# Kernel optimization log

Measured on AMD Instinct MI355X. Metric: run time of the kernel, lower is better.

Reference implementation:

```python
import jax, jax.numpy as jnp
import numpy as np
from functools import partial

B, S, D = 64, 1024, 1024
C = 10  # number of chained GRU steps (self.c)


def setup_inputs() -> dict:
    key = jax.random.key(0)
    ks = jax.random.split(key, 8)
    sc = 1.0 / np.sqrt(D)
    return {
        "feat": jax.random.normal(ks[0], (B, S, D), dtype=jnp.float32),
        "a_w": jax.random.normal(ks[1], (D,), dtype=jnp.float32) * sc,          # Linear(D,1,bias=False)
        "W_ih": jax.random.normal(ks[2], (3 * D, D + 1), dtype=jnp.float32) * sc,  # GRU input weights (r,z,n)
        "W_hh": jax.random.normal(ks[3], (3 * D, D), dtype=jnp.float32) * sc,      # GRU hidden weights (r,z,n)
        "b_ih": jax.random.normal(ks[4], (3 * D,), dtype=jnp.float32) * sc,
        "b_hh": jax.random.normal(ks[5], (3 * D,), dtype=jnp.float32) * sc,
        "W_out": jax.random.normal(ks[6], (1, D), dtype=jnp.float32) * sc,         # out_layer Linear(D,1)
        "b_out": jax.random.normal(ks[7], (1,), dtype=jnp.float32) * sc,
    }


def reference(feat, a_w, W_ih, W_hh, b_ih, b_hh, W_out, b_out):
    # Attention pooling: softmax over sequence dim of a scalar score per frame.
    logits = jnp.einsum("bsd,d->bs", feat, a_w)                 # [B, S]
    w = jax.nn.softmax(logits, axis=1)                           # [B, S]
    pooled = jnp.einsum("bs,bsd->bd", w, feat)                  # [B, D]

    def gru_step(carry, _):
        h, score = carry
        x = jnp.concatenate([pooled, score], axis=-1)            # [B, D+1]
        gi = x @ W_ih.T + b_ih                                   # [B, 3D]
        gh = h @ W_hh.T + b_hh                                   # [B, 3D]
        i_r, i_z, i_n = jnp.split(gi, 3, axis=-1)
        h_r, h_z, h_n = jnp.split(gh, 3, axis=-1)
        r = jax.nn.sigmoid(i_r + h_r)
        z = jax.nn.sigmoid(i_z + h_z)
        n = jnp.tanh(i_n + r * h_n)
        h_new = (1.0 - z) * n + z * h
        score_new = jax.nn.sigmoid(h_new @ W_out.T + b_out)      # [B, 1]
        return (h_new, score_new), score_new

    h0 = jnp.zeros_like(pooled)                                  # GRU hidden starts at zero
    s0 = jnp.zeros((pooled.shape[0], 1), dtype=pooled.dtype)     # zero_score initial chain input
    _, scores = jax.lax.scan(gru_step, (h0, s0), None, length=C)  # scores: [C, B, 1]
    out = jnp.transpose(scores[..., 0], (1, 0))                  # [B, C]
    return out
```

## Files before the change

### kernel.cpp

```cpp
#include <hip/hip_runtime.h>
#include <hip/hip_bf16.h>
#include <math.h>

#define B 64
#define S 1024
#define D 1024
#define C 10
#define TD 3072

typedef __attribute__((ext_vector_type(8))) short s8v;
typedef __attribute__((ext_vector_type(4))) float f4v;

__device__ __forceinline__ float wave_sum_bc(float v) {
    #pragma unroll
    for (int off = 1; off < 64; off <<= 1) v += __shfl_xor(v, off, 64);
    return v;
}
__device__ __forceinline__ float sigm(float x) { return 1.0f / (1.0f + expf(-x)); }
__device__ __forceinline__ short f2bf(float f) {
    __hip_bfloat16 h = __float2bfloat16(f);
    return *reinterpret_cast<short*>(&h);
}

__global__ __launch_bounds__(256) void k_pre(const float* __restrict__ feat,
        const float* __restrict__ a_w, const float* __restrict__ W_ih,
        const float* __restrict__ W_hh, float* __restrict__ part, float* __restrict__ ml,
        short* __restrict__ BihP, short* __restrict__ BhhP, float* __restrict__ wscore) {
    __shared__ float sacc[4][1024];
    __shared__ float sml[4][2];
    int n = blockIdx.x, tid = threadIdx.x;

    if (n >= 1024) {
        if (n < 4096) {
            int rel = n - 1024;
            const float* Wsrc = (rel < 1536) ? W_ih : W_hh;
            short* dst = (rel < 1536) ? BihP : BhhP;
            int stride = (rel < 1536) ? (D + 1) : D;
            int rn = (rel < 1536) ? rel : rel - 1536;
            int gid = rn * 256 + tid;
            int fid = gid >> 6, l = gid & 63;
            int s = fid & 31, g = (fid >> 5) % 3, dt = fid / 96;
            int row = g * 1024 + dt * 16 + (l & 15);
            int k0 = s * 32 + ((l >> 4) << 3);
            const float* src = Wsrc + (size_t)row * stride + k0;
            short v[8];
            #pragma unroll
            for (int j = 0; j < 8; ++j) v[j] = f2bf(src[j]);
            short* d = dst + ((size_t)fid * 64 + l) * 8;
            #pragma unroll
            for (int j = 0; j < 8; ++j) d[j] = v[j];
        } else {
            int j = (n - 4096) * 256 + tid;
            wscore[j] = W_ih[(size_t)j * (D + 1) + D];
        }
        return;
    }

    int ch = n & 15, b = n >> 4;
    int w = tid >> 6, lane = tid & 63;
    float4 aw[4], acc[4];
    #pragma unroll
    for (int r = 0; r < 4; ++r) {
        aw[r] = *reinterpret_cast<const float4*>(&a_w[r * 256 + lane * 4]);
        acc[r] = make_float4(0.f, 0.f, 0.f, 0.f);
    }
    float m = -INFINITY, l = 0.f;
    const float* fb = feat + ((size_t)b * S + ch * 64 + w * 16) * D;
    for (int i = 0; i < 16; ++i) {
        float4 f[4];
        #pragma unroll
        for (int r = 0; r < 4; ++r)
            f[r] = *reinterpret_cast<const float4*>(&fb[(size_t)i * D + r * 256 + lane * 4]);
        float dot = 0.f;
        #pragma unroll
        for (int r = 0; r < 4; ++r)
            dot += f[r].x * aw[r].x + f[r].y * aw[r].y + f[r].z * aw[r].z + f[r].w * aw[r].w;
        dot = wave_sum_bc(dot);
        if (dot <= m) {
            float wg = expf(dot - m);
            l += wg;
            #pragma unroll
            for (int r = 0; r < 4; ++r) {
                acc[r].x += wg * f[r].x; acc[r].y += wg * f[r].y;
                acc[r].z += wg * f[r].z; acc[r].w += wg * f[r].w;
            }
        } else {
            float sc = expf(m - dot);
            l = l * sc + 1.f;
            #pragma unroll
            for (int r = 0; r < 4; ++r) {
                acc[r].x = acc[r].x * sc + f[r].x; acc[r].y = acc[r].y * sc + f[r].y;
                acc[r].z = acc[r].z * sc + f[r].z; acc[r].w = acc[r].w * sc + f[r].w;
            }
            m = dot;
        }
    }
    #pragma unroll
    for (int r = 0; r < 4; ++r)
        *reinterpret_cast<float4*>(&sacc[w][r * 256 + lane * 4]) = acc[r];
    if (lane == 0) { sml[w][0] = m; sml[w][1] = l; }
    __syncthreads();
    float m0 = sml[0][0], m1 = sml[1][0], m2 = sml[2][0], m3 = sml[3][0];
    float mg = fmaxf(fmaxf(m0, m1), fmaxf(m2, m3));
    float s0 = expf(m0 - mg), s1 = expf(m1 - mg), s2 = expf(m2 - mg), s3 = expf(m3 - mg);
    int c = tid * 4;
    float4 a0 = *reinterpret_cast<float4*>(&sacc[0][c]);
    float4 a1 = *reinterpret_cast<float4*>(&sacc[1][c]);
    float4 a2 = *reinterpret_cast<float4*>(&sacc[2][c]);
    float4 a3 = *reinterpret_cast<float4*>(&sacc[3][c]);
    float4 o;
    o.x = s0 * a0.x + s1 * a1.x + s2 * a2.x + s3 * a3.x;
    o.y = s0 * a0.y + s1 * a1.y + s2 * a2.y + s3 * a3.y;
    o.z = s0 * a0.z + s1 * a1.z + s2 * a2.z + s3 * a3.z;
    o.w = s0 * a0.w + s1 * a1.w + s2 * a2.w + s3 * a3.w;
    *reinterpret_cast<float4*>(&part[((size_t)b * 16 + ch) * D + c]) = o;
    if (tid == 0) {
        float lg = s0 * sml[0][1] + s1 * sml[1][1] + s2 * sml[2][1] + s3 * sml[3][1];
        ml[(b * 16 + ch) * 2] = mg;
        ml[(b * 16 + ch) * 2 + 1] = lg;
    }
}

__global__ __launch_bounds__(256) void k_mid(const float* __restrict__ part,
        const float* __restrict__ ml, short* __restrict__ pooledP) {
    int b = blockIdx.x, tid = threadIdx.x;
    float mg = -INFINITY;
    #pragma unroll
    for (int q = 0; q < 16; ++q) mg = fmaxf(mg, ml[(b * 16 + q) * 2]);
    float denom = 0.f, sc[16];
    #pragma unroll
    for (int q = 0; q < 16; ++q) {
        sc[q] = expf(ml[(b * 16 + q) * 2] - mg);
        denom += sc[q] * ml[(b * 16 + q) * 2 + 1];
    }
    float inv = 1.f / denom;
    int c = tid * 4;
    float4 o = make_float4(0.f, 0.f, 0.f, 0.f);
    #pragma unroll
    for (int q = 0; q < 16; ++q) {
        float4 p = *reinterpret_cast<const float4*>(&part[((size_t)b * 16 + q) * D + c]);
        o.x += sc[q] * p.x; o.y += sc[q] * p.y; o.z += sc[q] * p.z; o.w += sc[q] * p.w;
    }
    float ov[4] = {o.x * inv, o.y * inv, o.z * inv, o.w * inv};
    int m = b >> 4;
    #pragma unroll
    for (int j4 = 0; j4 < 4; ++j4) {
        int d = c + j4;
        int s = d >> 5, lane2 = (b & 15) + (((d >> 3) & 3) << 4), jj = d & 7;
        pooledP[(((size_t)m * 32 + s) * 64 + lane2) * 8 + jj] = f2bf(ov[j4]);
    }
}

__global__ __launch_bounds__(512) void k_step(const s8v* __restrict__ Bp,
        const s8v* __restrict__ Ain, short* __restrict__ Aout, float* __restrict__ hf,
        float* __restrict__ gi0, const float* __restrict__ wscore,
        const float* __restrict__ b_ih, const float* __restrict__ b_hh,
        const float* __restrict__ W_out, const float* __restrict__ b_out,
        float* __restrict__ spart, float* __restrict__ out, int t) {
    __shared__ float psum[8][16][49];
    __shared__ float sredS[16][17];
    __shared__ float sredO[16][17];
    int tid = threadIdx.x, w = tid >> 6, l = tid & 63;
    int n = blockIdx.x, xcd = n & 7, slot = n >> 3;
    int dt = xcd * 8 + (slot & 7), bh = slot >> 3;
    int bq0 = bh * 16;
    int lb = tid & 15, c = (tid >> 4) & 15;
    bool epi = (tid < 256);
    int b = bq0 + lb, d = dt * 16 + c;

    float e_bo = 0.f, e_b0 = 0.f, e_b1 = 0.f, e_b2 = 0.f, e_wo = 0.f;
    float e_i0 = 0.f, e_i1 = 0.f, e_i2 = 0.f;
    float e_w0 = 0.f, e_w1 = 0.f, e_w2 = 0.f, e_hf = 0.f;
    if (epi) {
        e_bo = b_out[0];
        e_b0 = b_hh[d]; e_b1 = b_hh[D + d]; e_b2 = b_hh[2 * D + d];
        e_wo = W_out[d];
        if (t == 0) {
            e_i0 = b_ih[d]; e_i1 = b_ih[D + d]; e_i2 = b_ih[2 * D + d];
        } else {
            e_i0 = gi0[(size_t)b * TD + d];
            e_i1 = gi0[(size_t)b * TD + D + d];
            e_i2 = gi0[(size_t)b * TD + 2 * D + d];
            e_w0 = wscore[d]; e_w1 = wscore[D + d]; e_w2 = wscore[2 * D + d];
            e_hf = hf[(size_t)b * D + d];
            const float* sp = spart + ((size_t)(t - 1) * B + b) * 64 + c * 4;
            sredS[lb][c] = sp[0] + sp[1] + sp[2] + sp[3];
        }
    }

    f4v acc[3];
    #pragma unroll
    for (int g = 0; g < 3; ++g) acc[g] = (f4v){0.f, 0.f, 0.f, 0.f};
    #pragma unroll
    for (int s8 = 0; s8 < 4; ++s8) {
        int s = w * 4 + s8;
        s8v a  = Ain[((size_t)bh * 32 + s) * 64 + l];
        s8v b0 = Bp[((size_t)(dt * 3 + 0) * 32 + s) * 64 + l];
        s8v b1 = Bp[((size_t)(dt * 3 + 1) * 32 + s) * 64 + l];
        s8v b2 = Bp[((size_t)(dt * 3 + 2) * 32 + s) * 64 + l];
        acc[0] = __builtin_amdgcn_mfma_f32_16x16x32_bf16(a, b0, acc[0], 0, 0, 0);
        acc[1] = __builtin_amdgcn_mfma_f32_16x16x32_bf16(a, b1, acc[1], 0, 0, 0);
        acc[2] = __builtin_amdgcn_mfma_f32_16x16x32_bf16(a, b2, acc[2], 0, 0, 0);
    }
    #pragma unroll
    for (int g = 0; g < 3; ++g)
        #pragma unroll
        for (int r = 0; r < 4; ++r)
            psum[w][(l >> 4) * 4 + r][g * 16 + (l & 15)] = acc[g][r];
    __syncthreads();

    if (epi) {
        float g3[3];
        #pragma unroll
        for (int g = 0; g < 3; ++g) {
            int c48 = g * 16 + c;
            float v = 0.f;
            #pragma unroll
            for (int ww = 0; ww < 8; ++ww) v += psum[ww][lb][c48];
            g3[g] = v;
        }
        float gir, giz, gin, ghr, ghz, ghn, hprev;
        if (t == 0) {
            gir = g3[0] + e_i0;
            giz = g3[1] + e_i1;
            gin = g3[2] + e_i2;
            gi0[(size_t)b * TD + d] = gir;
            gi0[(size_t)b * TD + D + d] = giz;
            gi0[(size_t)b * TD + 2 * D + d] = gin;
            ghr = e_b0; ghz = e_b1; ghn = e_b2;
            hprev = 0.f;
        } else {
            float ssum = e_bo;
            #pragma unroll
            for (int q = 0; q < 16; ++q) ssum += sredS[lb][q];
            float score = sigm(ssum);
            if (dt == 0 && c == 0) out[b * C + (t - 1)] = score;
            gir = e_i0 + score * e_w0;
            giz = e_i1 + score * e_w1;
            gin = e_i2 + score * e_w2;
            ghr = e_b0 + g3[0];
            ghz = e_b1 + g3[1];
            ghn = e_b2 + g3[2];
            hprev = e_hf;
        }
        float rr = sigm(gir + ghr);
        float zz = sigm(giz + ghz);
        float nn = tanhf(gin + rr * ghn);
        float hnew = (1.f - zz) * nn + zz * hprev;
        hf[(size_t)b * D + d] = hnew;
        int s = d >> 5, lane2 = (b & 15) + (((d >> 3) & 3) << 4), jj = d & 7;
        Aout[(((size_t)bh * 32 + s) * 64 + lane2) * 8 + jj] = f2bf(hnew);
        sredO[lb][c] = hnew * e_wo;
    }
    __syncthreads();
    if (tid < 16) {
        float v = 0.f;
        #pragma unroll
        for (int q = 0; q < 16; ++q) v += sredO[tid][q];
        spart[((size_t)t * B + bq0 + tid) * 64 + dt] = v;
    }
}

__global__ void k_final(const float* __restrict__ spart, const float* __restrict__ b_out,
                        float* __restrict__ out) {
    int b = threadIdx.x;
    float s = b_out[0];
    const float* sp = spart + ((size_t)(C - 1) * B + b) * 64;
    #pragma unroll
    for (int k = 0; k < 64; ++k) s += sp[k];
    out[b * C + (C - 1)] = sigm(s);
}

extern "C" void kernel_launch(void* const* d_in, const int* in_sizes, int n_in,
                              void* d_out, int out_size, void* d_ws, size_t ws_size,
                              hipStream_t stream) {
    const float* feat  = (const float*)d_in[0];
    const float* a_w   = (const float*)d_in[1];
    const float* W_ih  = (const float*)d_in[2];
    const float* W_hh  = (const float*)d_in[3];
    const float* b_ih  = (const float*)d_in[4];
    const float* b_hh  = (const float*)d_in[5];
    const float* W_out = (const float*)d_in[6];
    const float* b_out = (const float*)d_in[7];
    float* out = (float*)d_out;
    float* ws = (float*)d_ws;

    float* part    = ws;
    float* ml      = part + (size_t)B * 16 * D;
    float* gi0     = ml + B * 16 * 2;
    float* hf      = gi0 + (size_t)B * TD;
    float* spart   = hf + B * D;
    float* wscore  = spart + (size_t)C * B * 64;
    short* pooledP = (short*)(wscore + TD);
    short* hpA     = pooledP + (size_t)B * D;
    short* hpB     = hpA + (size_t)B * D;
    short* BihP    = hpB + (size_t)B * D;
    short* BhhP    = BihP + (size_t)D * TD;

    k_pre<<<dim3(4108), 256, 0, stream>>>(feat, a_w, W_ih, W_hh, part, ml,
                                          BihP, BhhP, wscore);
    k_mid<<<dim3(64), 256, 0, stream>>>(part, ml, pooledP);
    k_step<<<dim3(256), 512, 0, stream>>>((const s8v*)BihP, (const s8v*)pooledP, hpA,
                                          hf, gi0, wscore, b_ih, b_hh, W_out, b_out,
                                          spart, out, 0);
    for (int t = 1; t < C; ++t) {
        short* ain = (t & 1) ? hpA : hpB;
        short* aout = (t & 1) ? hpB : hpA;
        k_step<<<dim3(256), 512, 0, stream>>>((const s8v*)BhhP, (const s8v*)ain, aout,
                                              hf, gi0, wscore, b_ih, b_hh, W_out, b_out,
                                              spart, out, t);
    }
    k_final<<<dim3(1), 64, 0, stream>>>(spart, b_out, out);
}
```

Before: 116.6 us.

## Fuse GRU step launches into one persistent kernel with atomic grid barriers

Replaces the ten per-step k_step launches and k_final with a single persistent kernel. Blocks synchronize through per-batch-group atomic counters and spin-wait instead of kernel boundaries. W_hh fragments stay in registers across steps, and gi and h stay in LDS instead of being reread from global memory. This removes launch overhead and repeated weight loads. It relies on all 256 blocks being co-resident and on relaxed atomics giving enough ordering, so it risks deadlock or stale reads.

```diff
diff --git a/kernel.cpp b/kernel.cpp
--- a/kernel.cpp
+++ b/kernel.cpp
@@ -10,6 +10,7 @@
 
 typedef __attribute__((ext_vector_type(8))) short s8v;
 typedef __attribute__((ext_vector_type(4))) float f4v;
+typedef unsigned long long u64;
 
 __device__ __forceinline__ float wave_sum_bc(float v) {
     #pragma unroll
@@ -21,11 +22,24 @@
     __hip_bfloat16 h = __float2bfloat16(f);
     return *reinterpret_cast<short*>(&h);
 }
+__device__ __forceinline__ u64 aload64(u64* p) {
+    return __hip_atomic_load(p, __ATOMIC_RELAXED, __HIP_MEMORY_SCOPE_AGENT);
+}
+__device__ __forceinline__ void astore64(u64* p, u64 v) {
+    __hip_atomic_store(p, v, __ATOMIC_RELAXED, __HIP_MEMORY_SCOPE_AGENT);
+}
+__device__ __forceinline__ float aloadf(float* p) {
+    return __hip_atomic_load(p, __ATOMIC_RELAXED, __HIP_MEMORY_SCOPE_AGENT);
+}
+__device__ __forceinline__ void astoref(float* p, float v) {
+    __hip_atomic_store(p, v, __ATOMIC_RELAXED, __HIP_MEMORY_SCOPE_AGENT);
+}
 
 __global__ __launch_bounds__(256) void k_pre(const float* __restrict__ feat,
         const float* __restrict__ a_w, const float* __restrict__ W_ih,
         const float* __restrict__ W_hh, float* __restrict__ part, float* __restrict__ ml,
-        short* __restrict__ BihP, short* __restrict__ BhhP, float* __restrict__ wscore) {
+        short* __restrict__ BihP, short* __restrict__ BhhP, float* __restrict__ wscore,
+        unsigned* __restrict__ bar) {
     __shared__ float sacc[4][1024];
     __shared__ float sml[4][2];
     int n = blockIdx.x, tid = threadIdx.x;
@@ -52,6 +66,7 @@
         } else {
             int j = (n - 4096) * 256 + tid;
             wscore[j] = W_ih[(size_t)j * (D + 1) + D];
+            if (n == 4096 && tid < 64) bar[tid] = 0u;
         }
         return;
     }
@@ -151,15 +166,19 @@
     }
 }
 
-__global__ __launch_bounds__(512) void k_step(const s8v* __restrict__ Bp,
-        const s8v* __restrict__ Ain, short* __restrict__ Aout, float* __restrict__ hf,
-        float* __restrict__ gi0, const float* __restrict__ wscore,
+__global__ __launch_bounds__(512, 2) void k_persist(const s8v* __restrict__ BihP,
+        const s8v* __restrict__ BhhP, const short* __restrict__ pooledP,
+        u64* hpA, u64* hpB, const float* __restrict__ wscore,
         const float* __restrict__ b_ih, const float* __restrict__ b_hh,
         const float* __restrict__ W_out, const float* __restrict__ b_out,
-        float* __restrict__ spart, float* __restrict__ out, int t) {
+        float* spart, float* __restrict__ out, unsigned* bar) {
     __shared__ float psum[8][16][49];
+    __shared__ float gilds[16][49];
+    __shared__ float hl[16][17];
     __shared__ float sredS[16][17];
     __shared__ float sredO[16][17];
+    __shared__ unsigned short hbf[16][16];
+
     int tid = threadIdx.x, w = tid >> 6, l = tid & 63;
     int n = blockIdx.x, xcd = n & 7, slot = n >> 3;
     int dt = xcd * 8 + (slot & 7), bh = slot >> 3;
@@ -167,108 +186,184 @@
     int lb = tid & 15, c = (tid >> 4) & 15;
     bool epi = (tid < 256);
     int b = bq0 + lb, d = dt * 16 + c;
-
-    float e_bo = 0.f, e_b0 = 0.f, e_b1 = 0.f, e_b2 = 0.f, e_wo = 0.f;
-    float e_i0 = 0.f, e_i1 = 0.f, e_i2 = 0.f;
-    float e_w0 = 0.f, e_w1 = 0.f, e_w2 = 0.f, e_hf = 0.f;
+    unsigned* cnt = &bar[bh * 16];
+
+    float e_bo = b_out[0];
+    float e_b0 = 0.f, e_b1 = 0.f, e_b2 = 0.f, e_wo = 0.f;
+    float e_w0 = 0.f, e_w1 = 0.f, e_w2 = 0.f;
     if (epi) {
-        e_bo = b_out[0];
         e_b0 = b_hh[d]; e_b1 = b_hh[D + d]; e_b2 = b_hh[2 * D + d];
         e_wo = W_out[d];
-        if (t == 0) {
-            e_i0 = b_ih[d]; e_i1 = b_ih[D + d]; e_i2 = b_ih[2 * D + d];
-        } else {
-            e_i0 = gi0[(size_t)b * TD + d];
-            e_i1 = gi0[(size_t)b * TD + D + d];
-            e_i2 = gi0[(size_t)b * TD + 2 * D + d];
-            e_w0 = wscore[d]; e_w1 = wscore[D + d]; e_w2 = wscore[2 * D + d];
-            e_hf = hf[(size_t)b * D + d];
-            const float* sp = spart + ((size_t)(t - 1) * B + b) * 64 + c * 4;
-            sredS[lb][c] = sp[0] + sp[1] + sp[2] + sp[3];
-        }
-    }
-
-    f4v acc[3];
-    #pragma unroll
-    for (int g = 0; g < 3; ++g) acc[g] = (f4v){0.f, 0.f, 0.f, 0.f};
+        e_w0 = wscore[d]; e_w1 = wscore[D + d]; e_w2 = wscore[2 * D + d];
+    }
+
+    s8v Bw[4][3];
     #pragma unroll
     for (int s8 = 0; s8 < 4; ++s8) {
         int s = w * 4 + s8;
-        s8v a  = Ain[((size_t)bh * 32 + s) * 64 + l];
-        s8v b0 = Bp[((size_t)(dt * 3 + 0) * 32 + s) * 64 + l];
-        s8v b1 = Bp[((size_t)(dt * 3 + 1) * 32 + s) * 64 + l];
-        s8v b2 = Bp[((size_t)(dt * 3 + 2) * 32 + s) * 64 + l];
-        acc[0] = __builtin_amdgcn_mfma_f32_16x16x32_bf16(a, b0, acc[0], 0, 0, 0);
-        acc[1] = __builtin_amdgcn_mfma_f32_16x16x32_bf16(a, b1, acc[1], 0, 0, 0);
-        acc[2] = __builtin_amdgcn_mfma_f32_16x16x32_bf16(a, b2, acc[2], 0, 0, 0);
-    }
-    #pragma unroll
-    for (int g = 0; g < 3; ++g)
-        #pragma unroll
-        for (int r = 0; r < 4; ++r)
-            psum[w][(l >> 4) * 4 + r][g * 16 + (l & 15)] = acc[g][r];
-    __syncthreads();
-
-    if (epi) {
-        float g3[3];
-        #pragma unroll
-        for (int g = 0; g < 3; ++g) {
-            int c48 = g * 16 + c;
+        #pragma unroll
+        for (int g = 0; g < 3; ++g)
+            Bw[s8][g] = BhhP[((size_t)(dt * 3 + g) * 32 + s) * 64 + l];
+    }
+
+    {
+        const s8v* Ap = reinterpret_cast<const s8v*>(pooledP);
+        f4v acc[3];
+        #pragma unroll
+        for (int g = 0; g < 3; ++g) acc[g] = (f4v){0.f, 0.f, 0.f, 0.f};
+        #pragma unroll
+        for (int s8 = 0; s8 < 4; ++s8) {
+            int s = w * 4 + s8;
+            s8v a = Ap[((size_t)bh * 32 + s) * 64 + l];
+            #pragma unroll
+            for (int g = 0; g < 3; ++g) {
+                s8v bb = BihP[((size_t)(dt * 3 + g) * 32 + s) * 64 + l];
+                acc[g] = __builtin_amdgcn_mfma_f32_16x16x32_bf16(a, bb, acc[g], 0, 0, 0);
+            }
+        }
+        #pragma unroll
+        for (int g = 0; g < 3; ++g)
+            #pragma unroll
+            for (int r = 0; r < 4; ++r)
+                psum[w][(l >> 4) * 4 + r][g * 16 + (l & 15)] = acc[g][r];
+        __syncthreads();
+        if (epi) {
+            float g3[3];
+            #pragma unroll
+            for (int g = 0; g < 3; ++g) {
+                float v = 0.f;
+                #pragma unroll
+                for (int ww = 0; ww < 8; ++ww) v += psum[ww][lb][g * 16 + c];
+                g3[g] = v;
+            }
+            float gir = g3[0] + b_ih[d];
+            float giz = g3[1] + b_ih[D + d];
+            float gin = g3[2] + b_ih[2 * D + d];
+            gilds[lb][c] = gir; gilds[lb][16 + c] = giz; gilds[lb][32 + c] = gin;
+            float rr = sigm(gir + e_b0);
+            float zz = sigm(giz + e_b1);
+            float nn = tanhf(gin + rr * e_b2);
+            float hnew = (1.f - zz) * nn;
+            hl[lb][c] = hnew;
+            hbf[lb][c] = (unsigned short)f2bf(hnew);
+            sredO[lb][c] = hnew * e_wo;
+        }
+        __syncthreads();
+        if (tid < 64) {
+            int lb2 = tid & 15, k4 = tid >> 4;
+            u64 v = (u64)hbf[lb2][k4 * 4] | ((u64)hbf[lb2][k4 * 4 + 1] << 16) |
+                    ((u64)hbf[lb2][k4 * 4 + 2] << 32) | ((u64)hbf[lb2][k4 * 4 + 3] << 48);
+            int q2 = (2 * dt + (k4 >> 1)) & 3;
+            int lane2 = lb2 + (q2 << 4);
+            size_t idx = (((size_t)bh * 32 + (dt >> 1)) * 64 + lane2) * 2 + (k4 & 1);
+            astore64(&hpA[idx], v);
+        }
+        if (tid < 16) {
             float v = 0.f;
             #pragma unroll
-            for (int ww = 0; ww < 8; ++ww) v += psum[ww][lb][c48];
-            g3[g] = v;
-        }
-        float gir, giz, gin, ghr, ghz, ghn, hprev;
-        if (t == 0) {
-            gir = g3[0] + e_i0;
-            giz = g3[1] + e_i1;
-            gin = g3[2] + e_i2;
-            gi0[(size_t)b * TD + d] = gir;
-            gi0[(size_t)b * TD + D + d] = giz;
-            gi0[(size_t)b * TD + 2 * D + d] = gin;
-            ghr = e_b0; ghz = e_b1; ghn = e_b2;
-            hprev = 0.f;
-        } else {
+            for (int q = 0; q < 16; ++q) v += sredO[tid][q];
+            astoref(&spart[((size_t)0 * B + bq0 + tid) * 64 + dt], v);
+        }
+        __syncthreads();
+        if (tid == 0)
+            __hip_atomic_fetch_add(cnt, 1u, __ATOMIC_RELAXED, __HIP_MEMORY_SCOPE_AGENT);
+    }
+
+    for (int t = 1; t < C; ++t) {
+        if (tid == 0) {
+            unsigned tgt = (unsigned)(t * 64);
+            while (__hip_atomic_load(cnt, __ATOMIC_RELAXED, __HIP_MEMORY_SCOPE_AGENT) < tgt)
+                __builtin_amdgcn_s_sleep(4);
+        }
+        __syncthreads();
+        if (epi) {
+            float* sp = &spart[((size_t)(t - 1) * B + b) * 64 + c * 4];
+            sredS[lb][c] = aloadf(sp) + aloadf(sp + 1) + aloadf(sp + 2) + aloadf(sp + 3);
+        }
+        u64* Ain = (t & 1) ? hpA : hpB;
+        u64* Aout = (t & 1) ? hpB : hpA;
+        f4v acc[3];
+        #pragma unroll
+        for (int g = 0; g < 3; ++g) acc[g] = (f4v){0.f, 0.f, 0.f, 0.f};
+        #pragma unroll
+        for (int s8 = 0; s8 < 4; ++s8) {
+            int s = w * 4 + s8;
+            size_t base = (((size_t)bh * 32 + s) * 64 + l) * 2;
+            union { u64 q[2]; s8v v; } au;
+            au.q[0] = aload64(&Ain[base]);
+            au.q[1] = aload64(&Ain[base + 1]);
+            #pragma unroll
+            for (int g = 0; g < 3; ++g)
+                acc[g] = __builtin_amdgcn_mfma_f32_16x16x32_bf16(au.v, Bw[s8][g], acc[g], 0, 0, 0);
+        }
+        #pragma unroll
+        for (int g = 0; g < 3; ++g)
+            #pragma unroll
+            for (int r = 0; r < 4; ++r)
+                psum[w][(l >> 4) * 4 + r][g * 16 + (l & 15)] = acc[g][r];
+        __syncthreads();
+        if (epi) {
+            float g3[3];
+            #pragma unroll
+            for (int g = 0; g < 3; ++g) {
+                float v = 0.f;
+                #pragma unroll
+                for (int ww = 0; ww < 8; ++ww) v += psum[ww][lb][g * 16 + c];
+                g3[g] = v;
+            }
             float ssum = e_bo;
             #pragma unroll
             for (int q = 0; q < 16; ++q) ssum += sredS[lb][q];
             float score = sigm(ssum);
             if (dt == 0 && c == 0) out[b * C + (t - 1)] = score;
-            gir = e_i0 + score * e_w0;
-            giz = e_i1 + score * e_w1;
-            gin = e_i2 + score * e_w2;
-            ghr = e_b0 + g3[0];
-            ghz = e_b1 + g3[1];
-            ghn = e_b2 + g3[2];
-            hprev = e_hf;
-        }
-        float rr = sigm(gir + ghr);
-        float zz = sigm(giz + ghz);
-        float nn = tanhf(gin + rr * ghn);
-        float hnew = (1.f - zz) * nn + zz * hprev;
-        hf[(size_t)b * D + d] = hnew;
-        int s = d >> 5, lane2 = (b & 15) + (((d >> 3) & 3) << 4), jj = d & 7;
-        Aout[(((size_t)bh * 32 + s) * 64 + lane2) * 8 + jj] = f2bf(hnew);
-        sredO[lb][c] = hnew * e_wo;
-    }
-    __syncthreads();
-    if (tid < 16) {
-        float v = 0.f;
-        #pragma unroll
-        for (int q = 0; q < 16; ++q) v += sredO[tid][q];
-        spart[((size_t)t * B + bq0 + tid) * 64 + dt] = v;
-    }
-}
-
-__global__ void k_final(const float* __restrict__ spart, const float* __restrict__ b_out,
-                        float* __restrict__ out) {
-    int b = threadIdx.x;
-    float s = b_out[0];
-    const float* sp = spart + ((size_t)(C - 1) * B + b) * 64;
-    #pragma unroll
-    for (int k = 0; k < 64; ++k) s += sp[k];
-    out[b * C + (C - 1)] = sigm(s);
+            float gir = gilds[lb][c]      + score * e_w0;
+            float giz = gilds[lb][16 + c] + score * e_w1;
+            float gin = gilds[lb][32 + c] + score * e_w2;
+            float rr = sigm(gir + e_b0 + g3[0]);
+            float zz = sigm(giz + e_b1 + g3[1]);
+            float nn = tanhf(gin + e_b2 + g3[2] + rr * (0.f) + rr * g3[2] * 0.f + 0.f);
+            nn = tanhf(gin + rr * (e_b2 + g3[2]));
+            float hnew = (1.f - zz) * nn + zz * hl[lb][c];
+            hl[lb][c] = hnew;
+            hbf[lb][c] = (unsigned short)f2bf(hnew);
+            sredO[lb][c] = hnew * e_wo;
+        }
+        __syncthreads();
+        if (tid < 64) {
+            int lb2 = tid & 15, k4 = tid >> 4;
+            u64 v = (u64)hbf[lb2][k4 * 4] | ((u64)hbf[lb2][k4 * 4 + 1] << 16) |
+                    ((u64)hbf[lb2][k4 * 4 + 2] << 32) | ((u64)hbf[lb2][k4 * 4 + 3] << 48);
+            int q2 = (2 * dt + (k4 >> 1)) & 3;
+            int lane2 = lb2 + (q2 << 4);
+            size_t idx = (((size_t)bh * 32 + (dt >> 1)) * 64 + lane2) * 2 + (k4 & 1);
+            astore64(&Aout[idx], v);
+        }
+        if (tid < 16) {
+            float v = 0.f;
+            #pragma unroll
+            for (int q = 0; q < 16; ++q) v += sredO[tid][q];
+            astoref(&spart[((size_t)t * B + bq0 + tid) * 64 + dt], v);
+        }
+        __syncthreads();
+        if (tid == 0)
+            __hip_atomic_fetch_add(cnt, 1u, __ATOMIC_RELAXED, __HIP_MEMORY_SCOPE_AGENT);
+    }
+
+    if (dt == 0) {
+        if (tid == 0) {
+            unsigned tgt = (unsigned)(C * 64);
+            while (__hip_atomic_load(cnt, __ATOMIC_RELAXED, __HIP_MEMORY_SCOPE_AGENT) < tgt)
+                __builtin_amdgcn_s_sleep(4);
+        }
+        __syncthreads();
+        if (tid < 16) {
+            int bb = bq0 + tid;
+            float s = e_bo;
+            for (int k = 0; k < 64; ++k)
+                s += aloadf(&spart[((size_t)(C - 1) * B + bb) * 64 + k]);
+            out[bb * C + (C - 1)] = sigm(s);
+        }
+    }
 }
 
 extern "C" void kernel_launch(void* const* d_in, const int* in_sizes, int n_in,
@@ -287,28 +382,20 @@
 
     float* part    = ws;
     float* ml      = part + (size_t)B * 16 * D;
-    float* gi0     = ml + B * 16 * 2;
-    float* hf      = gi0 + (size_t)B * TD;
-    float* spart   = hf + B * D;
+    float* spart   = ml + B * 16 * 2;
     float* wscore  = spart + (size_t)C * B * 64;
     short* pooledP = (short*)(wscore + TD);
     short* hpA     = pooledP + (size_t)B * D;
     short* hpB     = hpA + (size_t)B * D;
     short* BihP    = hpB + (size_t)B * D;
     short* BhhP    = BihP + (size_t)D * TD;
+    unsigned* bar  = (unsigned*)(BhhP + (size_t)D * TD);
 
     k_pre<<<dim3(4108), 256, 0, stream>>>(feat, a_w, W_ih, W_hh, part, ml,
-                                          BihP, BhhP, wscore);
+                                          BihP, BhhP, wscore, bar);
     k_mid<<<dim3(64), 256, 0, stream>>>(part, ml, pooledP);
-    k_step<<<dim3(256), 512, 0, stream>>>((const s8v*)BihP, (const s8v*)pooledP, hpA,
-                                          hf, gi0, wscore, b_ih, b_hh, W_out, b_out,
-                                          spart, out, 0);
-    for (int t = 1; t < C; ++t) {
-        short* ain = (t & 1) ? hpA : hpB;
-        short* aout = (t & 1) ? hpB : hpA;
-        k_step<<<dim3(256), 512, 0, stream>>>((const s8v*)BhhP, (const s8v*)ain, aout,
-                                              hf, gi0, wscore, b_ih, b_hh, W_out, b_out,
-                                              spart, out, t);
-    }
-    k_final<<<dim3(1), 64, 0, stream>>>(spart, b_out, out);
-}
+    k_persist<<<dim3(256), 512, 0, stream>>>((const s8v*)BihP, (const s8v*)BhhP,
+                                             pooledP, (u64*)hpA, (u64*)hpB,
+                                             wscore, b_ih, b_hh, W_out, b_out,
+                                             spart, out, bar);
+}
```

After: 111.9 us. 1.04x faster.
